# Performance work log

Hardware: AMD Instinct MI355X
Metric: run time of the kernel (lower is better)

The kernel has to match this reference:

```python
import jax, jax.numpy as jnp
import numpy as np

H = 64
EPS = 1e-8


def _quat_mul(q1, q2):
    w1, x1, y1, z1 = q1[..., 0], q1[..., 1], q1[..., 2], q1[..., 3]
    w2, x2, y2, z2 = q2[..., 0], q2[..., 1], q2[..., 2], q2[..., 3]
    return jnp.stack([
        w1 * w2 - x1 * x2 - y1 * y2 - z1 * z2,
        w1 * x2 + x1 * w2 + y1 * z2 - z1 * y2,
        w1 * y2 - x1 * z2 + y1 * w2 + z1 * x2,
        w1 * z2 + x1 * y2 - y1 * x2 + z1 * w2,
    ], axis=-1)


def _quat_conj(q):
    return q * jnp.array([1.0, -1.0, -1.0, -1.0], dtype=q.dtype)


def _oct_mul(o1, o2):
    # Cayley-Dickson: (a,b)(c,d) = (ac - conj(d) b, d a + b conj(c))
    a, b = o1[..., :4], o1[..., 4:]
    c, d = o2[..., :4], o2[..., 4:]
    re = _quat_mul(a, c) - _quat_mul(_quat_conj(d), b)
    im = _quat_mul(d, a) + _quat_mul(b, _quat_conj(c))
    return jnp.concatenate([re, im], axis=-1)


def setup_inputs() -> dict:
    key = jax.random.key(0)
    k0, k1, k2, k3, k4 = jax.random.split(key, 5)
    B, N, D = 16, 4096, H * 8
    o = jax.random.normal(k0, (B, N, D), dtype=jnp.float32)
    # scalar_mlp: Linear(2,32) -> GELU -> Linear(32,3), torch layout (out, in)
    W1 = jax.random.normal(k1, (32, 2), dtype=jnp.float32) * (1.0 / np.sqrt(2.0))
    b1 = jax.random.normal(k2, (32,), dtype=jnp.float32) * 0.01
    W2 = jax.random.normal(k3, (3, 32), dtype=jnp.float32) * (1.0 / np.sqrt(32.0))
    b2 = jax.random.normal(k4, (3,), dtype=jnp.float32) * 0.01
    alpha = jnp.asarray(0.25, dtype=jnp.float32)
    return {"o": o, "W1": W1, "b1": b1, "W2": W2, "b2": b2, "alpha": alpha}


def reference(o, W1, b1, W2, b2, alpha):
    B, N, D = o.shape
    oh = o.reshape(B, N, H, 8)                       # [B,N,H,8]
    r = oh[..., 0]                                   # real part [B,N,H]
    n = jnp.linalg.norm(oh[..., 1:], axis=-1)        # ||imag|| [B,N,H]
    inv = jnp.stack([r, n], axis=-1)                 # [B,N,H,2]
    h = jax.nn.gelu(inv @ W1.T + b1, approximate=False)
    scalars = h @ W2.T + b2                          # [B,N,H,3]
    a, b, c = scalars[..., 0], scalars[..., 1], scalars[..., 2]
    o2 = _oct_mul(oh, oh)
    o3 = _oct_mul(oh, o2)
    upd = a[..., None] * oh + b[..., None] * o2 + c[..., None] * o3
    upd = upd / jnp.maximum(jnp.linalg.norm(upd, axis=-1, keepdims=True), EPS)
    upd = upd.reshape(B, N, D)
    lam = jax.nn.sigmoid(alpha)
    return (1.0 - lam) * o + lam * upd
```

## Files before the change

kernel.cpp:

```cpp
#include <hip/hip_runtime.h>
#include <math.h>

#define OCT_EPS 1e-8f

__device__ __forceinline__ float fast_erf(float x) {
    float z = fabsf(x);
    float t = __builtin_amdgcn_rcpf(fmaf(0.3275911f, z, 1.0f));
    float p = fmaf(1.061405429f, t, -1.453152027f);
    p = fmaf(p, t, 1.421413741f);
    p = fmaf(p, t, -0.284496736f);
    p = fmaf(p, t, 0.254829592f);
    p = p * t;
    float e = __expf(-z * z);
    float r = fmaf(-p, e, 1.0f);
    return copysignf(r, x);
}

__device__ __forceinline__ float gelu_exact(float x) {
    return 0.5f * x * (1.0f + fast_erf(x * 0.70710678118654752f));
}

__global__ __launch_bounds__(256) void g2_ffn_kernel(
    const float* __restrict__ o,
    const float* __restrict__ W1,
    const float* __restrict__ b1,
    const float* __restrict__ W2,
    const float* __restrict__ b2,
    const float* __restrict__ alpha_p,
    float* __restrict__ out,
    int n_oct)
{
    int i = blockIdx.x * blockDim.x + threadIdx.x;
    if (i >= n_oct) return;

    const float4* ip = (const float4*)o;
    float4 lo = ip[2 * (size_t)i];
    float4 hi = ip[2 * (size_t)i + 1];

    float w = lo.x;
    float n2 = lo.y * lo.y;
    n2 = fmaf(lo.z, lo.z, n2);
    n2 = fmaf(lo.w, lo.w, n2);
    n2 = fmaf(hi.x, hi.x, n2);
    n2 = fmaf(hi.y, hi.y, n2);
    n2 = fmaf(hi.z, hi.z, n2);
    n2 = fmaf(hi.w, hi.w, n2);
    float n = __builtin_amdgcn_sqrtf(n2);
    float s = fmaf(w, w, n2);

    float a_acc = b2[0];
    float b_acc = b2[1];
    float c_acc = b2[2];
#pragma unroll
    for (int j = 0; j < 32; ++j) {
        float pre = fmaf(W1[2 * j], w, fmaf(W1[2 * j + 1], n, b1[j]));
        float h = gelu_exact(pre);
        a_acc = fmaf(W2[j], h, a_acc);
        b_acc = fmaf(W2[32 + j], h, b_acc);
        c_acc = fmaf(W2[64 + j], h, c_acc);
    }

    float alpha_c = fmaf(2.0f * b_acc, w, a_acc) + c_acc * fmaf(4.0f * w, w, -s);
    float beta_c  = -s * fmaf(2.0f * c_acc, w, b_acc);

    float t2 = fmaf(alpha_c * alpha_c, s,
               fmaf(2.0f * alpha_c * beta_c, w, beta_c * beta_c));
    float nrm = __builtin_amdgcn_sqrtf(t2);
    float inv = __builtin_amdgcn_rcpf(fmaxf(nrm, OCT_EPS));

    float alpha_in = alpha_p[0];
    float lam = 1.0f / (1.0f + __expf(-alpha_in));
    float oml = 1.0f - lam;

    float la = lam * alpha_c * inv;
    float lb = lam * beta_c * inv;

    float4 r0, r1;
    r0.x = fmaf(oml, lo.x, fmaf(la, lo.x, lb));
    r0.y = fmaf(oml, lo.y, la * lo.y);
    r0.z = fmaf(oml, lo.z, la * lo.z);
    r0.w = fmaf(oml, lo.w, la * lo.w);
    r1.x = fmaf(oml, hi.x, la * hi.x);
    r1.y = fmaf(oml, hi.y, la * hi.y);
    r1.z = fmaf(oml, hi.z, la * hi.z);
    r1.w = fmaf(oml, hi.w, la * hi.w);

    float4* op = (float4*)out;
    op[2 * (size_t)i]     = r0;
    op[2 * (size_t)i + 1] = r1;
}

extern "C" void kernel_launch(void* const* d_in, const int* in_sizes, int n_in,
                              void* d_out, int out_size, void* d_ws, size_t ws_size,
                              hipStream_t stream) {
    const float* o     = (const float*)d_in[0];
    const float* W1    = (const float*)d_in[1];
    const float* b1    = (const float*)d_in[2];
    const float* W2    = (const float*)d_in[3];
    const float* b2    = (const float*)d_in[4];
    const float* alpha = (const float*)d_in[5];
    float* out = (float*)d_out;

    int n_oct = in_sizes[0] / 8;
    int block = 256;
    int grid = (n_oct + block - 1) / block;
    g2_ffn_kernel<<<grid, block, 0, stream>>>(o, W1, b1, W2, b2, alpha, out, n_oct);
}
```

Measured before the change: 246.0 us.

## Process two octonions per thread using packed float2 math for the GELU MLP

Each thread now handles two octonions, one from each half of the array, and keeps them in 2-wide float vectors. This lets the compiler use packed FMA/MUL instructions (v_pk_fma_f32) for the 32-wide GELU MLP, which is the compute-heavy part. Transcendental ops stay scalar. It halves the thread count and raises register pressure per thread, which may lower occupancy for a kernel that is partly memory-bound.

```diff
diff --git a/kernel.cpp b/kernel.cpp
--- a/kernel.cpp
+++ b/kernel.cpp
@@ -3,21 +3,37 @@
 
 #define OCT_EPS 1e-8f
 
-__device__ __forceinline__ float fast_erf(float x) {
-    float z = fabsf(x);
-    float t = __builtin_amdgcn_rcpf(fmaf(0.3275911f, z, 1.0f));
-    float p = fmaf(1.061405429f, t, -1.453152027f);
-    p = fmaf(p, t, 1.421413741f);
-    p = fmaf(p, t, -0.284496736f);
-    p = fmaf(p, t, 0.254829592f);
-    p = p * t;
-    float e = __expf(-z * z);
-    float r = fmaf(-p, e, 1.0f);
-    return copysignf(r, x);
+typedef float v2f __attribute__((ext_vector_type(2)));
+typedef int   v2i __attribute__((ext_vector_type(2)));
+
+__device__ __forceinline__ v2f splat(float s) { v2f v; v.x = s; v.y = s; return v; }
+__device__ __forceinline__ v2i splati(int s)  { v2i v; v.x = s; v.y = s; return v; }
+__device__ __forceinline__ v2f vfma(v2f a, v2f b, v2f c) {
+    return __builtin_elementwise_fma(a, b, c);
 }
 
-__device__ __forceinline__ float gelu_exact(float x) {
-    return 0.5f * x * (1.0f + fast_erf(x * 0.70710678118654752f));
+__device__ __forceinline__ v2f gelu2(v2f x) {
+    v2i xi   = __builtin_bit_cast(v2i, x);
+    v2i sign = xi & splati(0x80000000);
+    v2f ax   = __builtin_bit_cast(v2f, xi ^ sign);
+    v2f z    = ax * splat(0.70710678118654752f);
+    v2f den  = vfma(z, splat(0.3275911f), splat(1.0f));
+    v2f t;
+    t.x = __builtin_amdgcn_rcpf(den.x);
+    t.y = __builtin_amdgcn_rcpf(den.y);
+    v2f p = vfma(splat(1.061405429f), t, splat(-1.453152027f));
+    p = vfma(p, t, splat(1.421413741f));
+    p = vfma(p, t, splat(-0.284496736f));
+    p = vfma(p, t, splat(0.254829592f));
+    p = p * t;
+    v2f nz2 = -(z * z);
+    v2f e;
+    e.x = __expf(nz2.x);
+    e.y = __expf(nz2.y);
+    v2f erf_abs = vfma(-p, e, splat(1.0f));
+    v2f er = __builtin_bit_cast(v2f, __builtin_bit_cast(v2i, erf_abs) | sign);
+    v2f hx = splat(0.5f) * x;
+    return vfma(hx, er, hx);
 }
 
 __global__ __launch_bounds__(256) void g2_ffn_kernel(
@@ -28,66 +44,96 @@
     const float* __restrict__ b2,
     const float* __restrict__ alpha_p,
     float* __restrict__ out,
-    int n_oct)
+    int n_oct, int half)
 {
     int i = blockIdx.x * blockDim.x + threadIdx.x;
-    if (i >= n_oct) return;
+    if (i >= half) return;
+
+    size_t i0 = (size_t)i;
+    size_t i1 = (size_t)i + half;
+    bool has1 = (i1 < (size_t)n_oct);
 
     const float4* ip = (const float4*)o;
-    float4 lo = ip[2 * (size_t)i];
-    float4 hi = ip[2 * (size_t)i + 1];
+    float4 aLo = ip[2 * i0];
+    float4 aHi = ip[2 * i0 + 1];
+    float4 bLo = has1 ? ip[2 * i1]     : aLo;
+    float4 bHi = has1 ? ip[2 * i1 + 1] : aHi;
 
-    float w = lo.x;
-    float n2 = lo.y * lo.y;
-    n2 = fmaf(lo.z, lo.z, n2);
-    n2 = fmaf(lo.w, lo.w, n2);
-    n2 = fmaf(hi.x, hi.x, n2);
-    n2 = fmaf(hi.y, hi.y, n2);
-    n2 = fmaf(hi.z, hi.z, n2);
-    n2 = fmaf(hi.w, hi.w, n2);
-    float n = __builtin_amdgcn_sqrtf(n2);
-    float s = fmaf(w, w, n2);
+    v2f w;  w.x  = aLo.x; w.y  = bLo.x;
+    v2f c1; c1.x = aLo.y; c1.y = bLo.y;
+    v2f c2; c2.x = aLo.z; c2.y = bLo.z;
+    v2f c3; c3.x = aLo.w; c3.y = bLo.w;
+    v2f c4; c4.x = aHi.x; c4.y = bHi.x;
+    v2f c5; c5.x = aHi.y; c5.y = bHi.y;
+    v2f c6; c6.x = aHi.z; c6.y = bHi.z;
+    v2f c7; c7.x = aHi.w; c7.y = bHi.w;
 
-    float a_acc = b2[0];
-    float b_acc = b2[1];
-    float c_acc = b2[2];
+    v2f n2 = c1 * c1;
+    n2 = vfma(c2, c2, n2);
+    n2 = vfma(c3, c3, n2);
+    n2 = vfma(c4, c4, n2);
+    n2 = vfma(c5, c5, n2);
+    n2 = vfma(c6, c6, n2);
+    n2 = vfma(c7, c7, n2);
+    v2f n;
+    n.x = __builtin_amdgcn_sqrtf(n2.x);
+    n.y = __builtin_amdgcn_sqrtf(n2.y);
+    v2f s = vfma(w, w, n2);
+
+    v2f a_acc = splat(b2[0]);
+    v2f b_acc = splat(b2[1]);
+    v2f c_acc = splat(b2[2]);
 #pragma unroll
     for (int j = 0; j < 32; ++j) {
-        float pre = fmaf(W1[2 * j], w, fmaf(W1[2 * j + 1], n, b1[j]));
-        float h = gelu_exact(pre);
-        a_acc = fmaf(W2[j], h, a_acc);
-        b_acc = fmaf(W2[32 + j], h, b_acc);
-        c_acc = fmaf(W2[64 + j], h, c_acc);
+        v2f pre = vfma(splat(W1[2 * j]), w,
+                  vfma(splat(W1[2 * j + 1]), n, splat(b1[j])));
+        v2f h = gelu2(pre);
+        a_acc = vfma(splat(W2[j]),      h, a_acc);
+        b_acc = vfma(splat(W2[32 + j]), h, b_acc);
+        c_acc = vfma(splat(W2[64 + j]), h, c_acc);
     }
 
-    float alpha_c = fmaf(2.0f * b_acc, w, a_acc) + c_acc * fmaf(4.0f * w, w, -s);
-    float beta_c  = -s * fmaf(2.0f * c_acc, w, b_acc);
+    v2f four_w2_s = vfma(splat(4.0f) * w, w, -s);
+    v2f alpha_c = vfma(splat(2.0f) * b_acc, w, a_acc) + c_acc * four_w2_s;
+    v2f beta_c  = -s * vfma(splat(2.0f) * c_acc, w, b_acc);
 
-    float t2 = fmaf(alpha_c * alpha_c, s,
-               fmaf(2.0f * alpha_c * beta_c, w, beta_c * beta_c));
-    float nrm = __builtin_amdgcn_sqrtf(t2);
-    float inv = __builtin_amdgcn_rcpf(fmaxf(nrm, OCT_EPS));
+    v2f t2 = vfma(alpha_c * alpha_c, s,
+             vfma(splat(2.0f) * alpha_c * beta_c, w, beta_c * beta_c));
+    v2f nrm;
+    nrm.x = __builtin_amdgcn_sqrtf(t2.x);
+    nrm.y = __builtin_amdgcn_sqrtf(t2.y);
+    v2f inv;
+    inv.x = __builtin_amdgcn_rcpf(fmaxf(nrm.x, OCT_EPS));
+    inv.y = __builtin_amdgcn_rcpf(fmaxf(nrm.y, OCT_EPS));
 
     float alpha_in = alpha_p[0];
     float lam = 1.0f / (1.0f + __expf(-alpha_in));
-    float oml = 1.0f - lam;
+    v2f vlam = splat(lam);
+    v2f oml  = splat(1.0f - lam);
 
-    float la = lam * alpha_c * inv;
-    float lb = lam * beta_c * inv;
+    v2f la = vlam * alpha_c * inv;
+    v2f lb = vlam * beta_c * inv;
 
-    float4 r0, r1;
-    r0.x = fmaf(oml, lo.x, fmaf(la, lo.x, lb));
-    r0.y = fmaf(oml, lo.y, la * lo.y);
-    r0.z = fmaf(oml, lo.z, la * lo.z);
-    r0.w = fmaf(oml, lo.w, la * lo.w);
-    r1.x = fmaf(oml, hi.x, la * hi.x);
-    r1.y = fmaf(oml, hi.y, la * hi.y);
-    r1.z = fmaf(oml, hi.z, la * hi.z);
-    r1.w = fmaf(oml, hi.w, la * hi.w);
+    v2f r0 = vfma(oml, w,  vfma(la, w,  lb));
+    v2f r1 = vfma(oml, c1, la * c1);
+    v2f r2 = vfma(oml, c2, la * c2);
+    v2f r3 = vfma(oml, c3, la * c3);
+    v2f r4 = vfma(oml, c4, la * c4);
+    v2f r5 = vfma(oml, c5, la * c5);
+    v2f r6 = vfma(oml, c6, la * c6);
+    v2f r7 = vfma(oml, c7, la * c7);
 
     float4* op = (float4*)out;
-    op[2 * (size_t)i]     = r0;
-    op[2 * (size_t)i + 1] = r1;
+    float4 oA0 = { r0.x, r1.x, r2.x, r3.x };
+    float4 oA1 = { r4.x, r5.x, r6.x, r7.x };
+    op[2 * i0]     = oA0;
+    op[2 * i0 + 1] = oA1;
+    if (has1) {
+        float4 oB0 = { r0.y, r1.y, r2.y, r3.y };
+        float4 oB1 = { r4.y, r5.y, r6.y, r7.y };
+        op[2 * i1]     = oB0;
+        op[2 * i1 + 1] = oB1;
+    }
 }
 
 extern "C" void kernel_launch(void* const* d_in, const int* in_sizes, int n_in,
@@ -102,7 +148,8 @@
     float* out = (float*)d_out;
 
     int n_oct = in_sizes[0] / 8;
+    int half = (n_oct + 1) / 2;
     int block = 256;
-    int grid = (n_oct + block - 1) / block;
-    g2_ffn_kernel<<<grid, block, 0, stream>>>(o, W1, b1, W2, b2, alpha, out, n_oct);
+    int grid = (half + block - 1) / block;
+    g2_ffn_kernel<<<grid, block, 0, stream>>>(o, W1, b1, W2, b2, alpha, out, n_oct, half);
 }
```

New measurement: 249.8 us. About the same (+1.5%).
